# Optimization experiments

Measured on AMD Instinct MI355X. Metric: run time of the kernel, lower is better.

The kernel has to match this reference:

```python
import jax, jax.numpy as jnp
import numpy as np

EPS = 1e-8

def setup_inputs() -> dict:
    key = jax.random.key(0)
    k1, k2, k3, k4 = jax.random.split(key, 4)
    b, in_c, out_c, style_c, k, h, w = 8, 512, 512, 512, 3, 64, 64
    return {
        "input": jax.random.normal(k1, (b, in_c, h, w), dtype=jnp.float32),
        "style": jax.random.normal(k2, (b, style_c), dtype=jnp.float32),
        "w_affine": jax.random.normal(k3, (in_c, style_c), dtype=jnp.float32),  # Linear weight, init N(0,1), runtime-scaled
        "b_affine": jnp.ones((1, in_c), dtype=jnp.float32),                     # Bias init_value=1.0
        "w_conv": jax.random.normal(k4, (out_c, in_c, k, k), dtype=jnp.float32),
    }

def reference(input, style, w_affine, b_affine, w_conv):
    b, in_c, h, w = input.shape
    out_c, _, kh, kw = w_conv.shape
    # Equalized-LR runtime scales (lr_mul=1):
    affine_scale = 1.0 / (w_affine.shape[1] ** 0.5)          # he_std for Linear
    conv_scale = 1.0 / ((in_c * kh * kw) ** 0.5)             # he_std for conv weight
    # affine: Linear + Bias (bias initialized to 1.0)
    s = style @ w_affine.T * affine_scale + b_affine          # [b, in_c]
    # modulate: per-sample weight tensor [b, out_c, in_c, kh, kw]
    wgt = s[:, None, :, None, None] * (w_conv * conv_scale)[None]
    # demodulate
    demod = jax.lax.rsqrt(jnp.sum(wgt * wgt, axis=(2, 3, 4), keepdims=True) + EPS)
    wgt = wgt * demod
    # grouped conv with groups = batch (stride=1, padding=1)
    x = input.reshape(1, b * in_c, h, w)
    wgt = wgt.reshape(b * out_c, in_c, kh, kw)
    out = jax.lax.conv_general_dilated(
        x, wgt,
        window_strides=(1, 1),
        padding=[(1, 1), (1, 1)],
        dimension_numbers=("NCHW", "OIHW", "NCHW"),
        feature_group_count=b,
    )
    return out.reshape(b, out_c, h, w)
```

## Files before the change

kernel.cpp:

```cpp
#include <hip/hip_runtime.h>
#include <hip/hip_bf16.h>

#define BB 8
#define CIN 512
#define COUT 512
#define HH 64
#define WW 64

#define AFF_SCALE 0.044194173824159216f
#define CONV_SCALE 0.014731391274719736f
#define CONV_SCALE2 (1.0f/4608.0f)

typedef short s16x8 __attribute__((ext_vector_type(8)));
typedef float f32x16 __attribute__((ext_vector_type(16)));

__device__ __forceinline__ unsigned short f2bf(float f) {
  __hip_bfloat16 h = __float2bfloat16(f);
  return *reinterpret_cast<unsigned short*>(&h);
}

__device__ __forceinline__ void gload_lds16(const void* g, void* l) {
  __builtin_amdgcn_global_load_lds(
      (const __attribute__((address_space(1))) unsigned int*)g,
      (__attribute__((address_space(3))) unsigned int*)l, 16, 0, 0);
}

__global__ __launch_bounds__(256) void affine_kernel(
    const float* __restrict__ style, const float* __restrict__ wa,
    const float* __restrict__ ba, float* __restrict__ smod) {
  int wid  = (blockIdx.x << 2) + (threadIdx.x >> 6);
  int lane = threadIdx.x & 63;
  int b  = wid >> 9;
  int ic = wid & 511;
  const float* s = style + b * CIN;
  const float* w = wa + (size_t)ic * CIN;
  float sum = 0.f;
#pragma unroll
  for (int k = 0; k < CIN / 64; ++k) sum += s[lane + 64 * k] * w[lane + 64 * k];
#pragma unroll
  for (int off = 32; off; off >>= 1) sum += __shfl_down(sum, off, 64);
  if (lane == 0) smod[wid] = sum * AFF_SCALE + ba[ic];
}

__global__ __launch_bounds__(256) void wsq_kernel(
    const float* __restrict__ wc, float* __restrict__ wsq) {
  int i = blockIdx.x * 256 + threadIdx.x;
  const float* p = wc + (size_t)i * 9;
  float s = 0.f;
#pragma unroll
  for (int k = 0; k < 9; ++k) { float v = p[k]; s += v * v; }
  wsq[i] = s;
}

__global__ __launch_bounds__(256) void demod_kernel(
    const float* __restrict__ smod, const float* __restrict__ wsq,
    float* __restrict__ demod) {
  int wid  = (blockIdx.x << 2) + (threadIdx.x >> 6);
  int lane = threadIdx.x & 63;
  int b  = wid >> 9;
  int oc = wid & 511;
  const float* s = smod + b * CIN;
  const float* w = wsq + (size_t)oc * CIN;
  float sum = 0.f;
#pragma unroll
  for (int k = 0; k < CIN / 64; ++k) {
    float sv = s[lane + 64 * k];
    sum += sv * sv * w[lane + 64 * k];
  }
#pragma unroll
  for (int off = 32; off; off >>= 1) sum += __shfl_down(sum, off, 64);
  if (lane == 0) demod[wid] = rsqrtf(sum * CONV_SCALE2 + 1e-8f) * CONV_SCALE;
}

__global__ __launch_bounds__(256) void premod_kernel(
    const float* __restrict__ xin, const float* __restrict__ smod,
    ushort* __restrict__ xt) {
  int n = blockIdx.x * 256 + threadIdx.x;
  int kg = n & 3;
  int x  = (n >> 2) & 63;
  int y  = (n >> 8) & 63;
  int g  = (n >> 14) & 15;
  int b  = n >> 18;
  int ic0 = g * 32 + kg * 8;
  const float* sp = smod + b * CIN + ic0;
  const float* xp = xin + (((size_t)b * CIN + ic0) * HH + y) * WW + x;
  s16x8 o;
#pragma unroll
  for (int j = 0; j < 8; ++j) {
    float v = xp[(size_t)j * HH * WW] * sp[j];
    o[j] = (short)f2bf(v);
  }
  *(s16x8*)(xt + (size_t)n * 8) = o;
}

__global__ __launch_bounds__(256) void wpack_kernel(
    const float* __restrict__ wc, ushort* __restrict__ wfrag) {
  int n = blockIdx.x * 256 + threadIdx.x;
  int l    = n & 63;
  int ks   = (n >> 6) & 1;
  int mf   = (n >> 7) & 15;
  int widx = n >> 11;
  int g = widx / 9, tap = widx % 9;
  int kh = tap / 3, kw = tap - kh * 3;
  int oc  = mf * 32 + (l & 31);
  int ic0 = g * 32 + ks * 16 + 8 * (l >> 5);
  s16x8 o;
#pragma unroll
  for (int j = 0; j < 8; ++j) {
    float v = wc[((size_t)oc * CIN + ic0 + j) * 9 + kh * 3 + kw];
    o[j] = (short)f2bf(v);
  }
  *(s16x8*)(wfrag + (size_t)n * 8) = o;
}

#define XS_ROW 4224
#define XS_BUF (6 * XS_ROW)

#define MFMA1(A_, B_, C_) __builtin_amdgcn_mfma_f32_32x32x16_bf16(A_, B_, C_, 0, 0, 0)

#define MH(W_, SX, SY, kf) \
  __builtin_amdgcn_s_setprio(1); \
  acc[0][0] = MFMA1(W_[0], SX[0 + (kf)], acc[0][0]); \
  acc[1][0] = MFMA1(W_[1], SX[0 + (kf)], acc[1][0]); \
  acc[0][1] = MFMA1(W_[0], SX[2 + (kf)], acc[0][1]); \
  acc[1][1] = MFMA1(W_[1], SX[2 + (kf)], acc[1][1]); \
  acc[0][2] = MFMA1(W_[0], SY[0 + (kf)], acc[0][2]); \
  acc[1][2] = MFMA1(W_[1], SY[0 + (kf)], acc[1][2]); \
  acc[0][3] = MFMA1(W_[0], SY[2 + (kf)], acc[0][3]); \
  acc[1][3] = MFMA1(W_[1], SY[2 + (kf)], acc[1][3]); \
  __builtin_amdgcn_s_setprio(0);

#define WPRE(W_, POFF, KS) \
  W_[0] = *(const s16x8*)(wg + (size_t)(POFF) * 32768 + (KS) * 1024); \
  W_[1] = *(const s16x8*)(wg + (size_t)(POFF) * 32768 + 2048 + (KS) * 1024);

#define LOADSLOT(S, RR, DXI) \
  S[0] = *(const s16x8*)(xs_r + (wr2 + (RR)) * XS_ROW + addrV[0][DXI][0]); \
  S[1] = *(const s16x8*)(xs_r + (wr2 + (RR)) * XS_ROW + addrV[0][DXI][1]); \
  S[2] = *(const s16x8*)(xs_r + (wr2 + (RR)) * XS_ROW + addrV[1][DXI][0]); \
  S[3] = *(const s16x8*)(xs_r + (wr2 + (RR)) * XS_ROW + addrV[1][DXI][1]);

#define GBARRIER \
  __builtin_amdgcn_sched_barrier(0); \
  asm volatile("s_waitcnt vmcnt(16)" ::: "memory"); \
  __builtin_amdgcn_sched_barrier(0); \
  __builtin_amdgcn_s_barrier(); \
  __builtin_amdgcn_sched_barrier(0);

#define GBODY(GG, E0, E1, O0, O1, TAILC) \
{ \
  const char* xs_r = (const char*)lds + (GG) * XS_BUF; \
  char* xs_w = lds + ((GG) ^ 1) * XS_BUF; \
  const char* wg = wl + (size_t)(g2 * 18 + (GG) * 9) * 32768; \
  LOADSLOT(bA, 0, 0) LOADSLOT(bB, 1, 0) \
   MH(E0, bA, bB, 0) WPRE(E0, 6, 0) LOADSLOT(bC, 2, 0) \
         MH(E1, bA, bB, 1) WPRE(E1, 6, 1) \
   MH(O0, bB, bC, 0) WPRE(O0, 1, 0) LOADSLOT(bA, 3, 0) \
         MH(O1, bB, bC, 1) WPRE(O1, 1, 1) \
   MH(E0, bC, bA, 0) WPRE(E0, 4, 0) LOADSLOT(bB, 0, 1) \
         MH(E1, bC, bA, 1) WPRE(E1, 4, 1) LOADSLOT(bC, 1, 1) \
   MH(O0, bB, bC, 0) WPRE(O0, 7, 0) LOADSLOT(bA, 2, 1) \
         MH(O1, bB, bC, 1) WPRE(O1, 7, 1) \
   MH(E0, bC, bA, 0) WPRE(E0, 2, 0) LOADSLOT(bB, 3, 1) \
         MH(E1, bC, bA, 1) WPRE(E1, 2, 1) \
   if (TAILC) stage6(xtb, (size_t)(b * 16 + g2 * 2 + (GG) + 1) * 262144, srcoff, xs_w, lds_woff, y0); \
         MH(O0, bA, bB, 0) WPRE(O0, 5, 0) LOADSLOT(bC, 0, 2) \
         MH(O1, bA, bB, 1) WPRE(O1, 5, 1) LOADSLOT(bA, 1, 2) \
   MH(E0, bC, bA, 0) WPRE(E0, 8, 0) LOADSLOT(bB, 2, 2) \
         MH(E1, bC, bA, 1) WPRE(E1, 8, 1) \
   MH(O0, bA, bB, 0) WPRE(O0, 9, 0) LOADSLOT(bC, 3, 2) \
         MH(O1, bA, bB, 1) WPRE(O1, 9, 1) \
   MH(E0, bB, bC, 0) WPRE(E0, 12, 0) \
         MH(E1, bB, bC, 1) WPRE(E1, 12, 1) \
  if (TAILC) { GBARRIER } \
}

__device__ __forceinline__ void stage6(const char* xtb, size_t gbase, int srcoff,
                                       char* xs_w, int lds_woff, int y0) {
  __builtin_amdgcn_sched_barrier(0);
#pragma unroll
  for (int r = 0; r < 6; ++r) {
    int gy = y0 - 1 + r;
    if (gy >= 0 && gy < HH)
      gload_lds16(xtb + gbase + (size_t)gy * 4096 + srcoff,
                  xs_w + r * XS_ROW + lds_woff);
  }
  __builtin_amdgcn_sched_barrier(0);
}

__global__ __launch_bounds__(256, 2) void conv_mfma(
    const ushort* __restrict__ xt,
    const ushort* __restrict__ wfrag,
    const float* __restrict__ demod,
    float* __restrict__ out) {
  __shared__ char lds[2 * XS_BUF];

  int tid = threadIdx.x;
  int l = tid & 63, w = tid >> 6;
  int wm = w >> 1, wr = w & 1;
  int wr2 = wr * 2;
  int bid = blockIdx.x;
  int ocb = bid & 3;
  int b   = (bid >> 2) & 7;
  int yt  = bid >> 5;
  int y0  = yt * 4;

  f32x16 acc[2][4];
#pragma unroll
  for (int i = 0; i < 2; ++i)
#pragma unroll
    for (int j = 0; j < 4; ++j)
#pragma unroll
      for (int e = 0; e < 16; ++e) acc[i][j][e] = 0.f;

  if (tid < 96) {
    int buf = tid & 1, side = (tid >> 1) & 1, kgz = (tid >> 2) & 3, r = tid >> 4;
    int chunk = side ? (260 + kgz) : kgz;
    *(int4*)(lds + buf * XS_BUF + r * XS_ROW + chunk * 16) = int4{0, 0, 0, 0};
  }
  if (y0 == 0) {
    for (int i = tid; i < 512; i += 256) {
      int buf = i & 1, chunk = 4 + (i >> 1);
      *(int4*)(lds + buf * XS_BUF + chunk * 16) = int4{0, 0, 0, 0};
    }
  }
  if (y0 == 60) {
    for (int i = tid; i < 512; i += 256) {
      int buf = i & 1, chunk = 4 + (i >> 1);
      *(int4*)(lds + buf * XS_BUF + 5 * XS_ROW + chunk * 16) = int4{0, 0, 0, 0};
    }
  }

  int addrV[2][3][2];
  {
    int lm = l & 31, kh2 = l >> 5;
#pragma unroll
    for (int ph = 0; ph < 2; ++ph)
#pragma unroll
      for (int dxi = 0; dxi < 3; ++dxi)
#pragma unroll
        for (int ks = 0; ks < 2; ++ks) {
          int col = ph * 32 + lm + dxi;
          int kg  = kh2 + 2 * ks;
          addrV[ph][dxi][ks] = (col * 4 + (kg ^ ((col >> 1) & 3))) * 16;
        }
  }

  int col_s = 1 + w * 16 + (l >> 2);
  int srcoff = (col_s - 1) * 64 + ((l & 3) ^ ((col_s >> 1) & 3)) * 16;
  int lds_woff = 64 + w * 1024;

  const char* xtb = (const char*)xt;
  const char* wl = (const char*)wfrag + (size_t)(ocb * 4 + wm * 2) * 2048 + (size_t)l * 16;

  s16x8 wHa[2], wHb[2], wHc[2], wHd[2];
  wHa[0] = *(const s16x8*)(wl);                       wHa[1] = *(const s16x8*)(wl + 2048);
  wHb[0] = *(const s16x8*)(wl + 1024);                wHb[1] = *(const s16x8*)(wl + 3072);
  wHc[0] = *(const s16x8*)(wl + 3 * 32768);           wHc[1] = *(const s16x8*)(wl + 3 * 32768 + 2048);
  wHd[0] = *(const s16x8*)(wl + 3 * 32768 + 1024);    wHd[1] = *(const s16x8*)(wl + 3 * 32768 + 3072);

  {
    size_t gbase = (size_t)(b * 16) * 262144;
#pragma unroll
    for (int r = 0; r < 6; ++r) {
      int gy = y0 - 1 + r;
      if (gy >= 0 && gy < HH)
        gload_lds16(xtb + gbase + (size_t)gy * 4096 + srcoff,
                    lds + r * XS_ROW + lds_woff);
    }
  }
  __syncthreads();

  s16x8 bA[4], bB[4], bC[4];

  for (int g2 = 0; g2 < 8; ++g2) {
    GBODY(0, wHa, wHb, wHc, wHd, true)
    GBODY(1, wHc, wHd, wHa, wHb, (g2 < 7))
  }

  int gy_base = y0 + wr2;
  int colbase = l & 31;
  int rowadd = 4 * (l >> 5);
#pragma unroll
  for (int q = 0; q < 2; ++q) {
#pragma unroll
    for (int reg = 0; reg < 16; ++reg) {
      int row = (reg & 3) + 8 * (reg >> 2) + rowadd;
      int oc = ocb * 128 + (wm * 2 + q) * 32 + row;
      float dm = demod[b * COUT + oc];
#pragma unroll
      for (int n = 0; n < 4; ++n) {
        int gy = gy_base + (n >> 1);
        int px = (n & 1) * 32 + colbase;
        out[((size_t)(b * COUT + oc)) * 4096 + gy * 64 + px] = acc[q][n][reg] * dm;
      }
    }
  }
}

extern "C" void kernel_launch(void* const* d_in, const int* in_sizes, int n_in,
                              void* d_out, int out_size, void* d_ws, size_t ws_size,
                              hipStream_t stream) {
  const float* input = (const float*)d_in[0];
  const float* style = (const float*)d_in[1];
  const float* wa    = (const float*)d_in[2];
  const float* ba    = (const float*)d_in[3];
  const float* wconv = (const float*)d_in[4];
  float* out = (float*)d_out;

  float* smod  = (float*)d_ws;
  float* demod = smod + BB * CIN;
  float* wsq   = demod + BB * COUT;
  ushort* wfrag = (ushort*)(wsq + (size_t)COUT * CIN);
  ushort* xt    = wfrag + (size_t)16 * 9 * 32 * 64 * 8;

  affine_kernel<<<BB * CIN / 4, 256, 0, stream>>>(style, wa, ba, smod);
  wsq_kernel<<<COUT * CIN / 256, 256, 0, stream>>>(wconv, wsq);
  demod_kernel<<<BB * COUT / 4, 256, 0, stream>>>(smod, wsq, demod);
  wpack_kernel<<<16 * 9 * 32 * 64 / 256, 256, 0, stream>>>(wconv, wfrag);
  premod_kernel<<<BB * 16 * 64 * 64 * 4 / 256, 256, 0, stream>>>(input, smod, xt);
  conv_mfma<<<BB * 4 * 16, 256, 0, stream>>>(xt, wfrag, demod, out);
}
```

Before: 152.8 us.

## Halve spatial tile to two output rows per block and raise occupancy

Each block now covers two output rows instead of four, so there are twice as many blocks (1024) and the per-wave accumulator drops from 8 to 4 MFMA tiles. The LDS input slab shrinks from 6 to 4 rows, and weight register buffers go from four to three sets in a rotating schedule, which lets launch bounds request 3 blocks per SM. The aim is more parallelism and better latency hiding. In exchange, each weight fragment is reused over half as many pixels, and the halo share rises, so more global and L2 traffic goes to weights and input rows.

```diff
diff --git a/kernel.cpp b/kernel.cpp
--- a/kernel.cpp
+++ b/kernel.cpp
@@ -114,31 +114,27 @@
 }
 
 #define XS_ROW 4224
-#define XS_BUF (6 * XS_ROW)
+#define XS_BUF (4 * XS_ROW)
 
 #define MFMA1(A_, B_, C_) __builtin_amdgcn_mfma_f32_32x32x16_bf16(A_, B_, C_, 0, 0, 0)
 
-#define MH(W_, SX, SY, kf) \
+#define MH(W_, S_, KF) \
   __builtin_amdgcn_s_setprio(1); \
-  acc[0][0] = MFMA1(W_[0], SX[0 + (kf)], acc[0][0]); \
-  acc[1][0] = MFMA1(W_[1], SX[0 + (kf)], acc[1][0]); \
-  acc[0][1] = MFMA1(W_[0], SX[2 + (kf)], acc[0][1]); \
-  acc[1][1] = MFMA1(W_[1], SX[2 + (kf)], acc[1][1]); \
-  acc[0][2] = MFMA1(W_[0], SY[0 + (kf)], acc[0][2]); \
-  acc[1][2] = MFMA1(W_[1], SY[0 + (kf)], acc[1][2]); \
-  acc[0][3] = MFMA1(W_[0], SY[2 + (kf)], acc[0][3]); \
-  acc[1][3] = MFMA1(W_[1], SY[2 + (kf)], acc[1][3]); \
+  acc[0][0] = MFMA1(W_[0], S_[0 + (KF)], acc[0][0]); \
+  acc[1][0] = MFMA1(W_[1], S_[0 + (KF)], acc[1][0]); \
+  acc[0][1] = MFMA1(W_[0], S_[2 + (KF)], acc[0][1]); \
+  acc[1][1] = MFMA1(W_[1], S_[2 + (KF)], acc[1][1]); \
   __builtin_amdgcn_s_setprio(0);
 
-#define WPRE(W_, POFF, KS) \
-  W_[0] = *(const s16x8*)(wg + (size_t)(POFF) * 32768 + (KS) * 1024); \
-  W_[1] = *(const s16x8*)(wg + (size_t)(POFF) * 32768 + 2048 + (KS) * 1024);
+#define WPRE(W_, TP, KS) \
+  W_[0] = *(const s16x8*)(wg + (size_t)(TP) * 32768 + (KS) * 1024); \
+  W_[1] = *(const s16x8*)(wg + (size_t)(TP) * 32768 + 2048 + (KS) * 1024);
 
 #define LOADSLOT(S, RR, DXI) \
-  S[0] = *(const s16x8*)(xs_r + (wr2 + (RR)) * XS_ROW + addrV[0][DXI][0]); \
-  S[1] = *(const s16x8*)(xs_r + (wr2 + (RR)) * XS_ROW + addrV[0][DXI][1]); \
-  S[2] = *(const s16x8*)(xs_r + (wr2 + (RR)) * XS_ROW + addrV[1][DXI][0]); \
-  S[3] = *(const s16x8*)(xs_r + (wr2 + (RR)) * XS_ROW + addrV[1][DXI][1]);
+  S[0] = *(const s16x8*)(xs_r + (wr + (RR)) * XS_ROW + addrV[0][DXI][0]); \
+  S[1] = *(const s16x8*)(xs_r + (wr + (RR)) * XS_ROW + addrV[0][DXI][1]); \
+  S[2] = *(const s16x8*)(xs_r + (wr + (RR)) * XS_ROW + addrV[1][DXI][0]); \
+  S[3] = *(const s16x8*)(xs_r + (wr + (RR)) * XS_ROW + addrV[1][DXI][1]);
 
 #define GBARRIER \
   __builtin_amdgcn_sched_barrier(0); \
@@ -147,39 +143,39 @@
   __builtin_amdgcn_s_barrier(); \
   __builtin_amdgcn_sched_barrier(0);
 
-#define GBODY(GG, E0, E1, O0, O1, TAILC) \
+#define GBODY(GG, TAILC) \
 { \
   const char* xs_r = (const char*)lds + (GG) * XS_BUF; \
   char* xs_w = lds + ((GG) ^ 1) * XS_BUF; \
   const char* wg = wl + (size_t)(g2 * 18 + (GG) * 9) * 32768; \
   LOADSLOT(bA, 0, 0) LOADSLOT(bB, 1, 0) \
-   MH(E0, bA, bB, 0) WPRE(E0, 6, 0) LOADSLOT(bC, 2, 0) \
-         MH(E1, bA, bB, 1) WPRE(E1, 6, 1) \
-   MH(O0, bB, bC, 0) WPRE(O0, 1, 0) LOADSLOT(bA, 3, 0) \
-         MH(O1, bB, bC, 1) WPRE(O1, 1, 1) \
-   MH(E0, bC, bA, 0) WPRE(E0, 4, 0) LOADSLOT(bB, 0, 1) \
-         MH(E1, bC, bA, 1) WPRE(E1, 4, 1) LOADSLOT(bC, 1, 1) \
-   MH(O0, bB, bC, 0) WPRE(O0, 7, 0) LOADSLOT(bA, 2, 1) \
-         MH(O1, bB, bC, 1) WPRE(O1, 7, 1) \
-   MH(E0, bC, bA, 0) WPRE(E0, 2, 0) LOADSLOT(bB, 3, 1) \
-         MH(E1, bC, bA, 1) WPRE(E1, 2, 1) \
-   if (TAILC) stage6(xtb, (size_t)(b * 16 + g2 * 2 + (GG) + 1) * 262144, srcoff, xs_w, lds_woff, y0); \
-         MH(O0, bA, bB, 0) WPRE(O0, 5, 0) LOADSLOT(bC, 0, 2) \
-         MH(O1, bA, bB, 1) WPRE(O1, 5, 1) LOADSLOT(bA, 1, 2) \
-   MH(E0, bC, bA, 0) WPRE(E0, 8, 0) LOADSLOT(bB, 2, 2) \
-         MH(E1, bC, bA, 1) WPRE(E1, 8, 1) \
-   MH(O0, bA, bB, 0) WPRE(O0, 9, 0) LOADSLOT(bC, 3, 2) \
-         MH(O1, bA, bB, 1) WPRE(O1, 9, 1) \
-   MH(E0, bB, bC, 0) WPRE(E0, 12, 0) \
-         MH(E1, bB, bC, 1) WPRE(E1, 12, 1) \
+   MH(wA, bA, 0) WPRE(wC, 3, 0) LOADSLOT(bC, 2, 0) \
+         MH(wB, bA, 1) WPRE(wA, 3, 1) \
+   MH(wC, bB, 0) WPRE(wB, 6, 0) LOADSLOT(bA, 0, 1) \
+         MH(wA, bB, 1) WPRE(wC, 6, 1) \
+   MH(wB, bC, 0) WPRE(wA, 1, 0) LOADSLOT(bB, 1, 1) \
+         MH(wC, bC, 1) WPRE(wB, 1, 1) \
+   MH(wA, bA, 0) WPRE(wC, 4, 0) LOADSLOT(bC, 2, 1) \
+         MH(wB, bA, 1) WPRE(wA, 4, 1) \
+   MH(wC, bB, 0) WPRE(wB, 7, 0) LOADSLOT(bA, 0, 2) \
+         MH(wA, bB, 1) WPRE(wC, 7, 1) \
+   if (TAILC) stage4(xtb, (size_t)(b * 16 + g2 * 2 + (GG) + 1) * 262144, srcoff, xs_w, lds_woff, y0); \
+         MH(wB, bC, 0) WPRE(wA, 2, 0) LOADSLOT(bB, 1, 2) \
+         MH(wC, bC, 1) WPRE(wB, 2, 1) \
+   MH(wA, bA, 0) WPRE(wC, 5, 0) LOADSLOT(bC, 2, 2) \
+         MH(wB, bA, 1) WPRE(wA, 5, 1) \
+   MH(wC, bB, 0) WPRE(wB, 8, 0) \
+         MH(wA, bB, 1) WPRE(wC, 8, 1) \
+   MH(wB, bC, 0) WPRE(wA, 9, 0) \
+         MH(wC, bC, 1) WPRE(wB, 9, 1) \
   if (TAILC) { GBARRIER } \
 }
 
-__device__ __forceinline__ void stage6(const char* xtb, size_t gbase, int srcoff,
+__device__ __forceinline__ void stage4(const char* xtb, size_t gbase, int srcoff,
                                        char* xs_w, int lds_woff, int y0) {
   __builtin_amdgcn_sched_barrier(0);
 #pragma unroll
-  for (int r = 0; r < 6; ++r) {
+  for (int r = 0; r < 4; ++r) {
     int gy = y0 - 1 + r;
     if (gy >= 0 && gy < HH)
       gload_lds16(xtb + gbase + (size_t)gy * 4096 + srcoff,
@@ -188,7 +184,7 @@
   __builtin_amdgcn_sched_barrier(0);
 }
 
-__global__ __launch_bounds__(256, 2) void conv_mfma(
+__global__ __launch_bounds__(256, 3) void conv_mfma(
     const ushort* __restrict__ xt,
     const ushort* __restrict__ wfrag,
     const float* __restrict__ demod,
@@ -198,36 +194,35 @@
   int tid = threadIdx.x;
   int l = tid & 63, w = tid >> 6;
   int wm = w >> 1, wr = w & 1;
-  int wr2 = wr * 2;
   int bid = blockIdx.x;
   int ocb = bid & 3;
   int b   = (bid >> 2) & 7;
   int yt  = bid >> 5;
-  int y0  = yt * 4;
-
-  f32x16 acc[2][4];
+  int y0  = yt * 2;
+
+  f32x16 acc[2][2];
 #pragma unroll
   for (int i = 0; i < 2; ++i)
 #pragma unroll
-    for (int j = 0; j < 4; ++j)
+    for (int j = 0; j < 2; ++j)
 #pragma unroll
       for (int e = 0; e < 16; ++e) acc[i][j][e] = 0.f;
 
-  if (tid < 96) {
-    int buf = tid & 1, side = (tid >> 1) & 1, kgz = (tid >> 2) & 3, r = tid >> 4;
+  if (tid < 64) {
+    int buf = tid & 1, side = (tid >> 1) & 1, kgz = (tid >> 2) & 3, r = (tid >> 4) & 3;
     int chunk = side ? (260 + kgz) : kgz;
     *(int4*)(lds + buf * XS_BUF + r * XS_ROW + chunk * 16) = int4{0, 0, 0, 0};
   }
   if (y0 == 0) {
-    for (int i = tid; i < 512; i += 256) {
-      int buf = i & 1, chunk = 4 + (i >> 1);
+    for (int i = tid; i < 528; i += 256) {
+      int buf = i & 1, chunk = i >> 1;
       *(int4*)(lds + buf * XS_BUF + chunk * 16) = int4{0, 0, 0, 0};
     }
   }
-  if (y0 == 60) {
-    for (int i = tid; i < 512; i += 256) {
-      int buf = i & 1, chunk = 4 + (i >> 1);
-      *(int4*)(lds + buf * XS_BUF + 5 * XS_ROW + chunk * 16) = int4{0, 0, 0, 0};
+  if (y0 == 62) {
+    for (int i = tid; i < 528; i += 256) {
+      int buf = i & 1, chunk = i >> 1;
+      *(int4*)(lds + buf * XS_BUF + 3 * XS_ROW + chunk * 16) = int4{0, 0, 0, 0};
     }
   }
 
@@ -253,16 +248,16 @@
   const char* xtb = (const char*)xt;
   const char* wl = (const char*)wfrag + (size_t)(ocb * 4 + wm * 2) * 2048 + (size_t)l * 16;
 
-  s16x8 wHa[2], wHb[2], wHc[2], wHd[2];
-  wHa[0] = *(const s16x8*)(wl);                       wHa[1] = *(const s16x8*)(wl + 2048);
-  wHb[0] = *(const s16x8*)(wl + 1024);                wHb[1] = *(const s16x8*)(wl + 3072);
-  wHc[0] = *(const s16x8*)(wl + 3 * 32768);           wHc[1] = *(const s16x8*)(wl + 3 * 32768 + 2048);
-  wHd[0] = *(const s16x8*)(wl + 3 * 32768 + 1024);    wHd[1] = *(const s16x8*)(wl + 3 * 32768 + 3072);
+  s16x8 wA[2], wB[2], wC[2];
+  wA[0] = *(const s16x8*)(wl);
+  wA[1] = *(const s16x8*)(wl + 2048);
+  wB[0] = *(const s16x8*)(wl + 1024);
+  wB[1] = *(const s16x8*)(wl + 3072);
 
   {
     size_t gbase = (size_t)(b * 16) * 262144;
 #pragma unroll
-    for (int r = 0; r < 6; ++r) {
+    for (int r = 0; r < 4; ++r) {
       int gy = y0 - 1 + r;
       if (gy >= 0 && gy < HH)
         gload_lds16(xtb + gbase + (size_t)gy * 4096 + srcoff,
@@ -274,11 +269,11 @@
   s16x8 bA[4], bB[4], bC[4];
 
   for (int g2 = 0; g2 < 8; ++g2) {
-    GBODY(0, wHa, wHb, wHc, wHd, true)
-    GBODY(1, wHc, wHd, wHa, wHb, (g2 < 7))
-  }
-
-  int gy_base = y0 + wr2;
+    GBODY(0, true)
+    GBODY(1, (g2 < 7))
+  }
+
+  int gy = y0 + wr;
   int colbase = l & 31;
   int rowadd = 4 * (l >> 5);
 #pragma unroll
@@ -288,12 +283,9 @@
       int row = (reg & 3) + 8 * (reg >> 2) + rowadd;
       int oc = ocb * 128 + (wm * 2 + q) * 32 + row;
       float dm = demod[b * COUT + oc];
-#pragma unroll
-      for (int n = 0; n < 4; ++n) {
-        int gy = gy_base + (n >> 1);
-        int px = (n & 1) * 32 + colbase;
-        out[((size_t)(b * COUT + oc)) * 4096 + gy * 64 + px] = acc[q][n][reg] * dm;
-      }
+      size_t obase = ((size_t)(b * COUT + oc)) * 4096 + gy * 64;
+      out[obase + colbase]      = acc[q][0][reg] * dm;
+      out[obase + 32 + colbase] = acc[q][1][reg] * dm;
     }
   }
 }
@@ -319,5 +311,5 @@
   demod_kernel<<<BB * COUT / 4, 256, 0, stream>>>(smod, wsq, demod);
   wpack_kernel<<<16 * 9 * 32 * 64 / 256, 256, 0, stream>>>(wconv, wfrag);
   premod_kernel<<<BB * 16 * 64 * 64 * 4 / 256, 256, 0, stream>>>(input, smod, xt);
-  conv_mfma<<<BB * 4 * 16, 256, 0, stream>>>(xt, wfrag, demod, out);
-}
+  conv_mfma<<<4 * BB * 32, 256, 0, stream>>>(xt, wfrag, demod, out);
+}
```

Result: slower. 175.0 us (+14.5%).

## Stage conv weights through triple-buffered LDS with per-tap barriers

Applied to the files above, without the earlier changes.

Weight fragments are no longer loaded by each wave straight from global memory into registers. The whole block now copies them into a three-slot LDS ring using async global-to-LDS loads, and each wave reads its A operands from LDS. This shares weight traffic between the two waves that use the same tiles and separates global latency from the MFMA loop. The cost is a block barrier with a vmcnt/lgkmcnt wait at every one of the nine taps, plus extra LDS footprint that may limit occupancy. The weight packing is also reordered to match the new tap order.

```diff
diff --git a/kernel.cpp b/kernel.cpp
--- a/kernel.cpp
+++ b/kernel.cpp
@@ -100,8 +100,8 @@
   int ks   = (n >> 6) & 1;
   int mf   = (n >> 7) & 15;
   int widx = n >> 11;
-  int g = widx / 9, tap = widx % 9;
-  int kh = tap / 3, kw = tap - kh * 3;
+  int g = widx / 9, p = widx % 9;
+  int kh = p % 3, kw = p / 3;
   int oc  = mf * 32 + (l & 31);
   int ic0 = g * 32 + ks * 16 + 8 * (l >> 5);
   s16x8 o;
@@ -115,24 +115,21 @@
 
 #define XS_ROW 4224
 #define XS_BUF (6 * XS_ROW)
+#define WS_BUFSZ 8192
 
 #define MFMA1(A_, B_, C_) __builtin_amdgcn_mfma_f32_32x32x16_bf16(A_, B_, C_, 0, 0, 0)
 
-#define MH(W_, SX, SY, kf) \
+#define MHK(KF, SX, SY) \
   __builtin_amdgcn_s_setprio(1); \
-  acc[0][0] = MFMA1(W_[0], SX[0 + (kf)], acc[0][0]); \
-  acc[1][0] = MFMA1(W_[1], SX[0 + (kf)], acc[1][0]); \
-  acc[0][1] = MFMA1(W_[0], SX[2 + (kf)], acc[0][1]); \
-  acc[1][1] = MFMA1(W_[1], SX[2 + (kf)], acc[1][1]); \
-  acc[0][2] = MFMA1(W_[0], SY[0 + (kf)], acc[0][2]); \
-  acc[1][2] = MFMA1(W_[1], SY[0 + (kf)], acc[1][2]); \
-  acc[0][3] = MFMA1(W_[0], SY[2 + (kf)], acc[0][3]); \
-  acc[1][3] = MFMA1(W_[1], SY[2 + (kf)], acc[1][3]); \
+  acc[0][0] = MFMA1(wA[KF],     SX[0 + (KF)], acc[0][0]); \
+  acc[1][0] = MFMA1(wA[2 + KF], SX[0 + (KF)], acc[1][0]); \
+  acc[0][1] = MFMA1(wA[KF],     SX[2 + (KF)], acc[0][1]); \
+  acc[1][1] = MFMA1(wA[2 + KF], SX[2 + (KF)], acc[1][1]); \
+  acc[0][2] = MFMA1(wA[KF],     SY[0 + (KF)], acc[0][2]); \
+  acc[1][2] = MFMA1(wA[2 + KF], SY[0 + (KF)], acc[1][2]); \
+  acc[0][3] = MFMA1(wA[KF],     SY[2 + (KF)], acc[0][3]); \
+  acc[1][3] = MFMA1(wA[2 + KF], SY[2 + (KF)], acc[1][3]); \
   __builtin_amdgcn_s_setprio(0);
-
-#define WPRE(W_, POFF, KS) \
-  W_[0] = *(const s16x8*)(wg + (size_t)(POFF) * 32768 + (KS) * 1024); \
-  W_[1] = *(const s16x8*)(wg + (size_t)(POFF) * 32768 + 2048 + (KS) * 1024);
 
 #define LOADSLOT(S, RR, DXI) \
   S[0] = *(const s16x8*)(xs_r + (wr2 + (RR)) * XS_ROW + addrV[0][DXI][0]); \
@@ -140,39 +137,52 @@
   S[2] = *(const s16x8*)(xs_r + (wr2 + (RR)) * XS_ROW + addrV[1][DXI][0]); \
   S[3] = *(const s16x8*)(xs_r + (wr2 + (RR)) * XS_ROW + addrV[1][DXI][1]);
 
-#define GBARRIER \
+#define ENTRYB \
   __builtin_amdgcn_sched_barrier(0); \
-  asm volatile("s_waitcnt vmcnt(16)" ::: "memory"); \
+  asm volatile("s_waitcnt vmcnt(2) lgkmcnt(0)" ::: "memory"); \
   __builtin_amdgcn_sched_barrier(0); \
   __builtin_amdgcn_s_barrier(); \
   __builtin_amdgcn_sched_barrier(0);
 
-#define GBODY(GG, E0, E1, O0, O1, TAILC) \
+#define AREAD(P) { \
+  const char* wsp_ = wsL + ((P) % 3) * WS_BUFSZ + aoff; \
+  wA[0] = *(const s16x8*)(wsp_); \
+  wA[1] = *(const s16x8*)(wsp_ + 1024); \
+  wA[2] = *(const s16x8*)(wsp_ + 2048); \
+  wA[3] = *(const s16x8*)(wsp_ + 3072); }
+
+#define WSISSUE(P) { \
+  const char* ws_s = wsg + (size_t)((P) + 2) * 32768; \
+  char* ws_d = wsdst + (((P) + 2) % 3) * WS_BUFSZ; \
+  gload_lds16(ws_s, ws_d); \
+  gload_lds16(ws_s + 4096, ws_d + 4096); }
+
+#define GBODY(GG, TAILC) \
 { \
   const char* xs_r = (const char*)lds + (GG) * XS_BUF; \
   char* xs_w = lds + ((GG) ^ 1) * XS_BUF; \
-  const char* wg = wl + (size_t)(g2 * 18 + (GG) * 9) * 32768; \
-  LOADSLOT(bA, 0, 0) LOADSLOT(bB, 1, 0) \
-   MH(E0, bA, bB, 0) WPRE(E0, 6, 0) LOADSLOT(bC, 2, 0) \
-         MH(E1, bA, bB, 1) WPRE(E1, 6, 1) \
-   MH(O0, bB, bC, 0) WPRE(O0, 1, 0) LOADSLOT(bA, 3, 0) \
-         MH(O1, bB, bC, 1) WPRE(O1, 1, 1) \
-   MH(E0, bC, bA, 0) WPRE(E0, 4, 0) LOADSLOT(bB, 0, 1) \
-         MH(E1, bC, bA, 1) WPRE(E1, 4, 1) LOADSLOT(bC, 1, 1) \
-   MH(O0, bB, bC, 0) WPRE(O0, 7, 0) LOADSLOT(bA, 2, 1) \
-         MH(O1, bB, bC, 1) WPRE(O1, 7, 1) \
-   MH(E0, bC, bA, 0) WPRE(E0, 2, 0) LOADSLOT(bB, 3, 1) \
-         MH(E1, bC, bA, 1) WPRE(E1, 2, 1) \
-   if (TAILC) stage6(xtb, (size_t)(b * 16 + g2 * 2 + (GG) + 1) * 262144, srcoff, xs_w, lds_woff, y0); \
-         MH(O0, bA, bB, 0) WPRE(O0, 5, 0) LOADSLOT(bC, 0, 2) \
-         MH(O1, bA, bB, 1) WPRE(O1, 5, 1) LOADSLOT(bA, 1, 2) \
-   MH(E0, bC, bA, 0) WPRE(E0, 8, 0) LOADSLOT(bB, 2, 2) \
-         MH(E1, bC, bA, 1) WPRE(E1, 8, 1) \
-   MH(O0, bA, bB, 0) WPRE(O0, 9, 0) LOADSLOT(bC, 3, 2) \
-         MH(O1, bA, bB, 1) WPRE(O1, 9, 1) \
-   MH(E0, bB, bC, 0) WPRE(E0, 12, 0) \
-         MH(E1, bB, bC, 1) WPRE(E1, 12, 1) \
-  if (TAILC) { GBARRIER } \
+  const char* wsg = wssrcb + (size_t)(g2 * 18 + (GG) * 9) * 32768; \
+   ENTRYB AREAD(0) \
+         LOADSLOT(bA, 0, 0) LOADSLOT(bB, 1, 0) \
+         WSISSUE(0) \
+         if (TAILC) stage6(xtb, (size_t)(b * 16 + g2 * 2 + (GG) + 1) * 262144, srcoff, xs_w, lds_woff, y0); \
+         MHK(0, bA, bB) LOADSLOT(bC, 2, 0) MHK(1, bA, bB) \
+   ENTRYB AREAD(1) WSISSUE(1) \
+         MHK(0, bB, bC) LOADSLOT(bA, 3, 0) MHK(1, bB, bC) \
+   ENTRYB AREAD(2) WSISSUE(2) \
+         MHK(0, bC, bA) LOADSLOT(bB, 0, 1) MHK(1, bC, bA) LOADSLOT(bC, 1, 1) \
+   ENTRYB AREAD(3) WSISSUE(3) \
+         MHK(0, bB, bC) LOADSLOT(bA, 2, 1) MHK(1, bB, bC) \
+   ENTRYB AREAD(4) WSISSUE(4) \
+         MHK(0, bC, bA) LOADSLOT(bB, 3, 1) MHK(1, bC, bA) \
+   ENTRYB AREAD(5) WSISSUE(5) \
+         MHK(0, bA, bB) LOADSLOT(bC, 0, 2) MHK(1, bA, bB) LOADSLOT(bA, 1, 2) \
+   ENTRYB AREAD(6) WSISSUE(6) \
+         MHK(0, bC, bA) LOADSLOT(bB, 2, 2) MHK(1, bC, bA) \
+   ENTRYB AREAD(7) WSISSUE(7) \
+         MHK(0, bA, bB) LOADSLOT(bC, 3, 2) MHK(1, bA, bB) \
+   ENTRYB AREAD(8) WSISSUE(8) \
+         MHK(0, bB, bC) MHK(1, bB, bC) \
 }
 
 __device__ __forceinline__ void stage6(const char* xtb, size_t gbase, int srcoff,
@@ -193,7 +203,7 @@
     const ushort* __restrict__ wfrag,
     const float* __restrict__ demod,
     float* __restrict__ out) {
-  __shared__ char lds[2 * XS_BUF];
+  __shared__ char lds[2 * XS_BUF + 3 * WS_BUFSZ];
 
   int tid = threadIdx.x;
   int l = tid & 63, w = tid >> 6;
@@ -205,6 +215,9 @@
   int yt  = bid >> 5;
   int y0  = yt * 4;
 
+  const char* wsL = (const char*)lds + 2 * XS_BUF;
+  char* wsdst = lds + 2 * XS_BUF + tid * 16;
+
   f32x16 acc[2][4];
 #pragma unroll
   for (int i = 0; i < 2; ++i)
@@ -251,13 +264,8 @@
   int lds_woff = 64 + w * 1024;
 
   const char* xtb = (const char*)xt;
-  const char* wl = (const char*)wfrag + (size_t)(ocb * 4 + wm * 2) * 2048 + (size_t)l * 16;
-
-  s16x8 wHa[2], wHb[2], wHc[2], wHd[2];
-  wHa[0] = *(const s16x8*)(wl);                       wHa[1] = *(const s16x8*)(wl + 2048);
-  wHb[0] = *(const s16x8*)(wl + 1024);                wHb[1] = *(const s16x8*)(wl + 3072);
-  wHc[0] = *(const s16x8*)(wl + 3 * 32768);           wHc[1] = *(const s16x8*)(wl + 3 * 32768 + 2048);
-  wHd[0] = *(const s16x8*)(wl + 3 * 32768 + 1024);    wHd[1] = *(const s16x8*)(wl + 3 * 32768 + 3072);
+  const char* wssrcb = (const char*)wfrag + (size_t)ocb * 8192 + (size_t)tid * 16;
+  int aoff = wm * 4096 + l * 16;
 
   {
     size_t gbase = (size_t)(b * 16) * 262144;
@@ -268,14 +276,18 @@
         gload_lds16(xtb + gbase + (size_t)gy * 4096 + srcoff,
                     lds + r * XS_ROW + lds_woff);
     }
-  }
-  __syncthreads();
-
+    gload_lds16(wssrcb,          wsdst);
+    gload_lds16(wssrcb + 4096,   wsdst + 4096);
+    gload_lds16(wssrcb + 32768,        wsdst + WS_BUFSZ);
+    gload_lds16(wssrcb + 32768 + 4096, wsdst + WS_BUFSZ + 4096);
+  }
+
+  s16x8 wA[4];
   s16x8 bA[4], bB[4], bC[4];
 
   for (int g2 = 0; g2 < 8; ++g2) {
-    GBODY(0, wHa, wHb, wHc, wHd, true)
-    GBODY(1, wHc, wHd, wHa, wHb, (g2 < 7))
+    GBODY(0, true)
+    GBODY(1, (g2 < 7))
   }
 
   int gy_base = y0 + wr2;
```

New measurement: 152.3 us. Within noise of the previous version (-0.4%).
